# Kernel tuning notes

Hardware: AMD Instinct MI355X
Metric: run time of the kernel (lower is better)

## Reference

```python
import itertools
import jax, jax.numpy as jnp
import numpy as np

ORDER = 3  # MaskDE(order=3) -> DescartesExtension orders 2..3
D = 80
B = 8192


def setup_inputs() -> dict:
    key = jax.random.key(0)
    kx, km = jax.random.split(key)
    x = jax.random.normal(kx, (B, D), dtype=jnp.float32)
    mask = jax.random.randint(km, (D,), 0, 2).astype(jnp.bool_)
    return {"x": x, "mask": mask}


def _comb_indices(m: int, order: int) -> np.ndarray:
    # combinations with replacement of range(m), shape (n_comb, order)
    return np.array(list(itertools.combinations_with_replacement(range(m), order)), dtype=np.int32)


def reference(x, mask):
    # mask is a concrete bool vector: masked_select == static gather
    idx = np.flatnonzero(np.asarray(mask))  # (m,)
    m = idx.size
    xm = x[:, idx]  # (B, m)
    parts = [xm]
    for order in range(2, ORDER + 1):
        combs = _comb_indices(m, order)           # (C, order)
        # gather-multiply-reduce: prod of each feature combination
        parts.append(jnp.prod(xm[:, combs], axis=-1))  # (B, C)
    return jnp.concatenate(parts, axis=-1)
```

## Files before the change

### kernel.cpp

```cpp
#include <hip/hip_runtime.h>
#include <stdint.h>

#define DMAX 80
#define BLK  256
#define XW   96
#define EPB  4096

typedef float f32x4 __attribute__((ext_vector_type(4)));

__global__ void maskde_setup(const void* __restrict__ mask_raw, int m,
                             int* __restrict__ idx_out,
                             uint16_t* __restrict__ pair16,
                             uint32_t* __restrict__ coltab,
                             int tpad, int T, int P) {
    int tid = blockIdx.x * blockDim.x + threadIdx.x;

    if (tid == 0) {
        const uint8_t* b8  = (const uint8_t*)mask_raw;
        const int*     b32 = (const int*)mask_raw;
        const float*   bf  = (const float*)mask_raw;
        int cnt = 0; bool ok = true;
        for (int i = 0; i < DMAX; ++i) { uint8_t v = b8[i]; if (v > 1) ok = false; cnt += (v != 0); }
        int mode;
        if (ok && cnt == m) {
            mode = 0;
        } else {
            cnt = 0; ok = true;
            for (int i = 0; i < DMAX; ++i) { int v = b32[i]; if (v != 0 && v != 1) ok = false; cnt += (v != 0); }
            mode = (ok && cnt == m) ? 1 : 2;
        }
        int k = 0;
        for (int i = 0; i < DMAX && k < m; ++i) {
            bool on = (mode == 0) ? (b8[i] != 0)
                    : (mode == 1) ? (b32[i] != 0)
                                  : (bf[i] != 0.0f);
            if (on) idx_out[k++] = i;
        }
    }

    int stride = gridDim.x * blockDim.x;
    for (int p = tid; p < P; p += stride) {
        int rem = p, i = 0;
        while (rem >= m - i) { rem -= (m - i); ++i; }
        int j = i + rem;

        pair16[p] = (uint16_t)(i | (j << 8));

        #define WR4(c, v) do {                                              \
            int _c = (c); uint32_t _v = (v);                                \
            coltab[_c] = _v;                                                \
            if (_c >= 1) coltab[tpad     + _c - 1] = _v;                    \
            if (_c >= 2) coltab[2 * tpad + _c - 2] = _v;                    \
            if (_c >= 3) coltab[3 * tpad + _c - 3] = _v;                    \
        } while (0)

        if (p < m)
            WR4(p, (uint32_t)P | ((uint32_t)p << 16));
        WR4(m + p, (uint32_t)p | ((uint32_t)m << 16));

        int mi = m - i;
        long long Si  = ((long long)m * (m + 1) * (m + 2)
                       - (long long)mi * (mi + 1) * (mi + 2)) / 6;
        int Rij = ((m - i) + (m - j + 1)) * (j - i) / 2;
        int base = m + P + (int)Si + Rij;
        for (int k3 = j; k3 < m; ++k3)
            WR4(base + (k3 - j), (uint32_t)p | ((uint32_t)k3 << 16));
        #undef WR4
    }
}

__global__ void maskde_xsel(const float* __restrict__ x,
                            const int* __restrict__ idx,
                            float* __restrict__ xsel, int m, int rows) {
    int g = blockIdx.x * BLK + threadIdx.x;
    int total = rows * XW;
    for (; g < total; g += gridDim.x * BLK) {
        int row = g / XW, k = g - row * XW;
        xsel[g] = (k < m) ? x[row * DMAX + idx[k]] : 1.0f;
    }
}

__global__ __launch_bounds__(BLK) void
maskde_expand(const float* __restrict__ xsel,
              const uint16_t* __restrict__ pair16,
              const uint32_t* __restrict__ coltab, int tpad,
              float* __restrict__ out, int m, int T, int P,
              int rows, int total) {
    extern __shared__ float sm[];
    float* xls0 = sm;
    float* xls1 = sm + XW;
    float* pps0 = sm + 2 * XW;
    float* pps1 = pps0 + (P + 1);

    const int tid = threadIdx.x;
    const int e0  = blockIdx.x * EPB;
    const int r0  = e0 / T;
    const int r0start = r0 * T;
    const bool has1 = (r0 + 1 < rows);

    if (tid < XW) {
        xls0[tid] = xsel[r0 * XW + tid];
    } else if (tid >= 128 && tid < 128 + XW) {
        int k = tid - 128;
        xls1[k] = has1 ? xsel[(r0 + 1) * XW + k] : 1.0f;
    }
    __syncthreads();

    for (int p = tid; p <= P; p += BLK) {
        float v0 = 1.0f, v1 = 1.0f;
        if (p < P) {
            uint32_t ij = pair16[p];
            int i = ij & 0xFF, j = (ij >> 8) & 0xFF;
            v0 = xls0[i] * xls0[j];
            v1 = xls1[i] * xls1[j];
        }
        pps0[p] = v0;
        pps1[p] = v1;
    }
    __syncthreads();

#pragma unroll
    for (int it = 0; it < EPB / (4 * BLK); ++it) {
        int ee = e0 + (tid << 2) + it * (4 * BLK);
        if (ee >= total) break;
        int c = ee - r0start;
        const float* pS = pps0;
        const float* xS = xls0;
        if (c >= T) { c -= T; pS = pps1; xS = xls1; }

        if (c <= T - 4 && ee + 3 < total) {
            int s = c & 3;
            const uint4* tp = (const uint4*)(coltab + (size_t)s * tpad + (c - s));
            uint4 t = *tp;
            f32x4 o;
            o.x = pS[t.x & 0xFFFF] * xS[t.x >> 16];
            o.y = pS[t.y & 0xFFFF] * xS[t.y >> 16];
            o.z = pS[t.z & 0xFFFF] * xS[t.z >> 16];
            o.w = pS[t.w & 0xFFFF] * xS[t.w >> 16];
            *(f32x4*)(out + ee) = o;
        } else {
            for (int u = 0; u < 4; ++u) {
                int e2 = ee + u;
                if (e2 >= total) break;
                int c2 = e2 - r0start;
                const float* p2 = pps0;
                const float* x2 = xls0;
                if (c2 >= T) { c2 -= T; p2 = pps1; x2 = xls1; }
                uint32_t en = coltab[c2];
                out[e2] = p2[en & 0xFFFF] * x2[en >> 16];
            }
        }
    }
}

extern "C" void kernel_launch(void* const* d_in, const int* in_sizes, int n_in,
                              void* d_out, int out_size, void* d_ws, size_t ws_size,
                              hipStream_t stream) {
    const float* x    = (const float*)d_in[0];
    const void*  mask = d_in[1];
    float*       out  = (float*)d_out;

    int rows = in_sizes[0] / DMAX;
    if (rows <= 0 || out_size <= 0) return;
    long long Tll = (long long)out_size / rows;

    int m = -1;
    for (int mm = 0; mm <= DMAX; ++mm) {
        long long t = (long long)mm
                    + (long long)mm * (mm + 1) / 2
                    + (long long)mm * (mm + 1) * (mm + 2) / 6;
        if (t == Tll) { m = mm; break; }
    }
    if (m <= 0) return;

    int T    = (int)Tll;
    int P    = m * (m + 1) / 2;
    int tpad = (T + 3) & ~3;
    int total = rows * T;

    int*      idx    = (int*)d_ws;
    uint16_t* pair16 = (uint16_t*)((char*)d_ws + 1024);
    uint32_t* coltab = (uint32_t*)((char*)d_ws + 32768);
    float*    xsel   = (float*)((char*)d_ws + 32768
                                + (size_t)4 * tpad * 4 + 256);

    int sblocks = (P + 255) / 256;
    if (sblocks < 1) sblocks = 1;
    maskde_setup<<<sblocks, 256, 0, stream>>>(mask, m, idx, pair16, coltab,
                                              tpad, T, P);

    int xblocks = (rows * XW + BLK - 1) / BLK;
    if (xblocks > 2048) xblocks = 2048;
    maskde_xsel<<<xblocks, BLK, 0, stream>>>(x, idx, xsel, m, rows);

    int nb = (total + EPB - 1) / EPB;
    size_t shmem = (size_t)(2 * XW + 2 * (P + 1)) * sizeof(float);
    maskde_expand<<<nb, BLK, shmem, stream>>>(xsel, pair16, coltab, tpad,
                                              out, m, T, P, rows, total);
}
```

Baseline: 127.6 us.

## Precompute per-row pair products globally and use a grid-stride expand kernel

Adds a separate kernel that computes every row's pairwise products into a global workspace buffer. The expand kernel becomes a grid-stride loop over quads that gathers directly from global memory, no longer building per-block shared-memory tables. The aim is to remove the shared-memory setup and the two barriers repeated in every block. The cost is an extra launch, tens of MB of extra global write and read traffic, and gathers served by the caches instead of LDS.

```diff
diff --git a/kernel.cpp b/kernel.cpp
--- a/kernel.cpp
+++ b/kernel.cpp
@@ -4,7 +4,7 @@
 #define DMAX 80
 #define BLK  256
 #define XW   96
-#define EPB  4096
+#define GRID 2048
 
 typedef float f32x4 __attribute__((ext_vector_type(4)));
 
@@ -80,72 +80,62 @@
     }
 }
 
+__global__ void maskde_ppsall(const float* __restrict__ xsel,
+                              const uint16_t* __restrict__ pair16,
+                              float* __restrict__ ppsall,
+                              int P, int PPS) {
+    int p   = blockIdx.x * BLK + threadIdx.x;
+    int row = blockIdx.y;
+    if (p > P) return;
+    float v = 1.0f;
+    if (p < P) {
+        uint32_t ij = pair16[p];
+        const float* xr = xsel + row * XW;
+        v = xr[ij & 0xFF] * xr[(ij >> 8) & 0xFF];
+    }
+    ppsall[(size_t)row * PPS + p] = v;
+}
+
 __global__ __launch_bounds__(BLK) void
 maskde_expand(const float* __restrict__ xsel,
-              const uint16_t* __restrict__ pair16,
+              const float* __restrict__ ppsall,
               const uint32_t* __restrict__ coltab, int tpad,
-              float* __restrict__ out, int m, int T, int P,
-              int rows, int total) {
-    extern __shared__ float sm[];
-    float* xls0 = sm;
-    float* xls1 = sm + XW;
-    float* pps0 = sm + 2 * XW;
-    float* pps1 = pps0 + (P + 1);
+              float* __restrict__ out, int T, int PPS,
+              int total, unsigned long long magicM) {
+    const int nquads = total >> 2;
+    const int gsz    = (int)gridDim.x * BLK;
 
-    const int tid = threadIdx.x;
-    const int e0  = blockIdx.x * EPB;
-    const int r0  = e0 / T;
-    const int r0start = r0 * T;
-    const bool has1 = (r0 + 1 < rows);
+    for (int q = blockIdx.x * BLK + threadIdx.x; q < nquads; q += gsz) {
+        int e = q << 2;
+        int row = (int)(((unsigned long long)e * magicM) >> 40);
+        int c = e - row * T;
+        if (c < 0)       { --row; c += T; }
+        else if (c >= T) { ++row; c -= T; }
 
-    if (tid < XW) {
-        xls0[tid] = xsel[r0 * XW + tid];
-    } else if (tid >= 128 && tid < 128 + XW) {
-        int k = tid - 128;
-        xls1[k] = has1 ? xsel[(r0 + 1) * XW + k] : 1.0f;
-    }
-    __syncthreads();
+        const float* pr = ppsall + (size_t)row * PPS;
+        const float* xr = xsel + row * XW;
 
-    for (int p = tid; p <= P; p += BLK) {
-        float v0 = 1.0f, v1 = 1.0f;
-        if (p < P) {
-            uint32_t ij = pair16[p];
-            int i = ij & 0xFF, j = (ij >> 8) & 0xFF;
-            v0 = xls0[i] * xls0[j];
-            v1 = xls1[i] * xls1[j];
-        }
-        pps0[p] = v0;
-        pps1[p] = v1;
-    }
-    __syncthreads();
-
-#pragma unroll
-    for (int it = 0; it < EPB / (4 * BLK); ++it) {
-        int ee = e0 + (tid << 2) + it * (4 * BLK);
-        if (ee >= total) break;
-        int c = ee - r0start;
-        const float* pS = pps0;
-        const float* xS = xls0;
-        if (c >= T) { c -= T; pS = pps1; xS = xls1; }
-
-        if (c <= T - 4 && ee + 3 < total) {
+        if (c <= T - 4) {
             int s = c & 3;
-            const uint4* tp = (const uint4*)(coltab + (size_t)s * tpad + (c - s));
-            uint4 t = *tp;
+            uint4 t = *(const uint4*)(coltab + (size_t)s * tpad + (c - s));
             f32x4 o;
-            o.x = pS[t.x & 0xFFFF] * xS[t.x >> 16];
-            o.y = pS[t.y & 0xFFFF] * xS[t.y >> 16];
-            o.z = pS[t.z & 0xFFFF] * xS[t.z >> 16];
-            o.w = pS[t.w & 0xFFFF] * xS[t.w >> 16];
-            *(f32x4*)(out + ee) = o;
+            o.x = pr[t.x & 0xFFFF] * xr[t.x >> 16];
+            o.y = pr[t.y & 0xFFFF] * xr[t.y >> 16];
+            o.z = pr[t.z & 0xFFFF] * xr[t.z >> 16];
+            o.w = pr[t.w & 0xFFFF] * xr[t.w >> 16];
+            *(f32x4*)(out + e) = o;
         } else {
             for (int u = 0; u < 4; ++u) {
-                int e2 = ee + u;
+                int e2 = e + u;
                 if (e2 >= total) break;
-                int c2 = e2 - r0start;
-                const float* p2 = pps0;
-                const float* x2 = xls0;
-                if (c2 >= T) { c2 -= T; p2 = pps1; x2 = xls1; }
+                int c2 = e2 - row * T;
+                const float* p2 = pr;
+                const float* x2 = xr;
+                if (c2 >= T) {
+                    c2 -= T;
+                    p2 = ppsall + (size_t)(row + 1) * PPS;
+                    x2 = xsel + (row + 1) * XW;
+                }
                 uint32_t en = coltab[c2];
                 out[e2] = p2[en & 0xFFFF] * x2[en >> 16];
             }
@@ -173,16 +163,23 @@
     }
     if (m <= 0) return;
 
-    int T    = (int)Tll;
-    int P    = m * (m + 1) / 2;
-    int tpad = (T + 3) & ~3;
+    int T     = (int)Tll;
+    int P     = m * (m + 1) / 2;
+    int PPS   = P + 1;
+    int tpad  = (T + 3) & ~3;
     int total = rows * T;
+    unsigned long long magicM = (1ULL << 40) / (unsigned long long)T + 1;
 
-    int*      idx    = (int*)d_ws;
-    uint16_t* pair16 = (uint16_t*)((char*)d_ws + 1024);
-    uint32_t* coltab = (uint32_t*)((char*)d_ws + 32768);
-    float*    xsel   = (float*)((char*)d_ws + 32768
-                                + (size_t)4 * tpad * 4 + 256);
+    char* ws = (char*)d_ws;
+    int*      idx    = (int*)ws;
+    uint16_t* pair16 = (uint16_t*)(ws + 1024);
+    uint32_t* coltab = (uint32_t*)(ws + 32768);
+    size_t off_xsel  = 32768 + (size_t)4 * tpad * 4 + 256;
+    off_xsel = (off_xsel + 255) & ~(size_t)255;
+    float*    xsel   = (float*)(ws + off_xsel);
+    size_t off_pps   = off_xsel + (size_t)rows * XW * 4;
+    off_pps = (off_pps + 255) & ~(size_t)255;
+    float*    ppsall = (float*)(ws + off_pps);
 
     int sblocks = (P + 255) / 256;
     if (sblocks < 1) sblocks = 1;
@@ -193,8 +190,9 @@
     if (xblocks > 2048) xblocks = 2048;
     maskde_xsel<<<xblocks, BLK, 0, stream>>>(x, idx, xsel, m, rows);
 
-    int nb = (total + EPB - 1) / EPB;
-    size_t shmem = (size_t)(2 * XW + 2 * (P + 1)) * sizeof(float);
-    maskde_expand<<<nb, BLK, shmem, stream>>>(xsel, pair16, coltab, tpad,
-                                              out, m, T, P, rows, total);
+    dim3 pgrid((PPS + BLK - 1) / BLK, rows);
+    maskde_ppsall<<<pgrid, BLK, 0, stream>>>(xsel, pair16, ppsall, P, PPS);
+
+    maskde_expand<<<GRID, BLK, 0, stream>>>(xsel, ppsall, coltab, tpad,
+                                            out, T, PPS, total, magicM);
 }
```

Measured after the change: 213.9 us. 67.6% more time.
